# Performance work log

Measured on AMD Instinct MI355X. Metric: run time of the kernel, lower is better.

The kernel has to match this reference:

```python
import jax, jax.numpy as jnp
import numpy as np

N = 100000   # nodes
E = 1600000  # edges (before self-loops)
IN, HID, OUT = 256, 128, 64
NEG_SLOPE = 0.2  # PyG GATConv default


def setup_inputs() -> dict:
    key = jax.random.key(0)
    ks = jax.random.split(key, 12)
    s = 0.05
    return {
        "x": jax.random.normal(ks[0], (N, IN), jnp.float32),
        "edge_index": jax.random.randint(ks[1], (2, E), 0, N, dtype=jnp.int32),
        "W1": jax.random.normal(ks[2], (IN, HID), jnp.float32) * s,
        "a1_src": jax.random.normal(ks[3], (HID,), jnp.float32) * s,
        "a1_dst": jax.random.normal(ks[4], (HID,), jnp.float32) * s,
        "b1": jnp.zeros((HID,), jnp.float32),
        "W2": jax.random.normal(ks[5], (HID, OUT), jnp.float32) * s,
        "a2_src": jax.random.normal(ks[6], (OUT,), jnp.float32) * s,
        "a2_dst": jax.random.normal(ks[7], (OUT,), jnp.float32) * s,
        "b2": jnp.zeros((OUT,), jnp.float32),
    }


def _gat_conv(x, src, dst, W, a_src, a_dst, b):
    """Single-head PyG GATConv (concat=True, heads=1), self-loops already in src/dst."""
    h = x @ W                                   # [N, F]
    alpha_s = h @ a_src                         # [N]
    alpha_d = h @ a_dst                         # [N]
    e = jax.nn.leaky_relu(alpha_s[src] + alpha_d[dst], NEG_SLOPE)  # [E+N]
    # segment softmax over edges grouped by destination node
    m = jax.ops.segment_max(e, dst, num_segments=N)                # [N]
    ex = jnp.exp(e - m[dst])
    denom = jax.ops.segment_sum(ex, dst, num_segments=N)           # [N]
    coef = ex / denom[dst]                                         # [E+N]
    out = jax.ops.segment_sum(h[src] * coef[:, None], dst, num_segments=N)
    return out + b


def reference(x, edge_index, W1, a1_src, a1_dst, b1, W2, a2_src, a2_dst, b2):
    loops = jnp.arange(N, dtype=edge_index.dtype)
    src = jnp.concatenate([edge_index[0], loops])
    dst = jnp.concatenate([edge_index[1], loops])
    h = _gat_conv(x, src, dst, W1, a1_src, a1_dst, b1)
    h = jax.nn.relu(h)
    # dropout is identity at inference (training=False)
    out = _gat_conv(h, src, dst, W2, a2_src, a2_dst, b2)
    return out
```

## Files before the change

kernel.cpp:

```cpp
#include <hip/hip_runtime.h>
#include <hip/hip_bf16.h>
#include <cstdint>

#define N_NODES 100000
#define N_EDGES 1600000
#define F_IN 256
#define F_HID 128
#define F_OUT 64
#define NEG_SLOPE 0.2f

#define BSH 7
#define NB 782
#define CAP 3072
#define CAPS 3072
#define NBLK_E 256

typedef __attribute__((ext_vector_type(8))) short bf16x8;
typedef __attribute__((ext_vector_type(4))) float f32x4;

__device__ __forceinline__ ushort f2bf(float f) {
  uint u = __float_as_uint(f);
  u += 0x7fffu + ((u >> 16) & 1u);
  return (ushort)(u >> 16);
}
__device__ __forceinline__ float bf2f(ushort s) {
  return __uint_as_float(((uint)s) << 16);
}
__device__ __forceinline__ uint pack2(float a, float b) {
  return (uint)f2bf(a) | ((uint)f2bf(b) << 16);
}

__global__ void wprep_kernel(const float* __restrict__ W, ushort* __restrict__ Wt,
                             int K, int Ncol) {
  int i = blockIdx.x * blockDim.x + threadIdx.x;
  if (i < K * Ncol) {
    int k = i / Ncol, c = i % Ncol;
    Wt[(size_t)c * K + k] = f2bf(W[i]);
  }
}

template <int BN, int K, bool AF32>
__global__ __launch_bounds__(256) void gemm_mfma(
    const void* __restrict__ Ap, const ushort* __restrict__ Bt,
    ushort* __restrict__ Cb, const float* __restrict__ a_src,
    const float* __restrict__ a_dst, float* __restrict__ as_,
    float* __restrict__ ad_, int M) {
  constexpr int CT = BN / 16;
  __shared__ __align__(16) ushort Alds[128 * 32];
  __shared__ __align__(16) ushort Blds[BN * 32];
  const int tid = threadIdx.x;
  const int wave = tid >> 6, lane = tid & 63;
  const int lr = lane & 15, lq = lane >> 4;
  const int gm0 = blockIdx.x * 128;

  f32x4 acc[2][CT];
#pragma unroll
  for (int a = 0; a < 2; ++a)
#pragma unroll
    for (int b = 0; b < CT; ++b)
#pragma unroll
      for (int e = 0; e < 4; ++e) acc[a][b][e] = 0.f;

  for (int kt = 0; kt < K; kt += 32) {
#pragma unroll
    for (int i = 0; i < 2; ++i) {
      int sid = i * 256 + tid;
      int row = sid >> 2, q = sid & 3;
      int gm = gm0 + row;
      uint4 w = make_uint4(0u, 0u, 0u, 0u);
      if (gm < M) {
        if (AF32) {
          const float* s = (const float*)Ap + (size_t)gm * K + kt + q * 8;
          float4 u = *(const float4*)s;
          float4 v = *(const float4*)(s + 4);
          w.x = pack2(u.x, u.y); w.y = pack2(u.z, u.w);
          w.z = pack2(v.x, v.y); w.w = pack2(v.z, v.w);
        } else {
          w = *(const uint4*)((const ushort*)Ap + (size_t)gm * K + kt + q * 8);
        }
      }
      int phys = row * 4 + (q ^ ((row >> 2) & 3));
      *(uint4*)&Alds[phys * 8] = w;
    }
#pragma unroll
    for (int i = 0; i < BN * 4 / 256; ++i) {
      int sid = i * 256 + tid;
      int row = sid >> 2, q = sid & 3;
      uint4 w = *(const uint4*)(Bt + (size_t)row * K + kt + q * 8);
      int phys = row * 4 + (q ^ ((row >> 2) & 3));
      *(uint4*)&Blds[phys * 8] = w;
    }
    __syncthreads();

    bf16x8 af[2], bfr[CT];
#pragma unroll
    for (int rt = 0; rt < 2; ++rt) {
      int r = wave * 32 + rt * 16 + lr;
      af[rt] = *(const bf16x8*)&Alds[(r * 4 + (lq ^ ((r >> 2) & 3))) * 8];
    }
#pragma unroll
    for (int c = 0; c < CT; ++c) {
      int r = c * 16 + lr;
      bfr[c] = *(const bf16x8*)&Blds[(r * 4 + (lq ^ ((r >> 2) & 3))) * 8];
    }
#pragma unroll
    for (int rt = 0; rt < 2; ++rt)
#pragma unroll
      for (int c = 0; c < CT; ++c)
        acc[rt][c] = __builtin_amdgcn_mfma_f32_16x16x32_bf16(af[rt], bfr[c], acc[rt][c], 0, 0, 0);
    __syncthreads();
  }

#pragma unroll
  for (int rt = 0; rt < 2; ++rt)
#pragma unroll
    for (int ri = 0; ri < 4; ++ri) {
      int gr = gm0 + wave * 32 + rt * 16 + lq * 4 + ri;
      if (gr < M) {
#pragma unroll
        for (int c = 0; c < CT; ++c)
          Cb[(size_t)gr * BN + c * 16 + lr] = f2bf(acc[rt][c][ri]);
      }
    }

  float avs[CT], avd[CT];
#pragma unroll
  for (int c = 0; c < CT; ++c) {
    avs[c] = a_src[c * 16 + lr];
    avd[c] = a_dst[c * 16 + lr];
  }
#pragma unroll
  for (int rt = 0; rt < 2; ++rt)
#pragma unroll
    for (int ri = 0; ri < 4; ++ri) {
      int gr = gm0 + wave * 32 + rt * 16 + lq * 4 + ri;
      float s = 0.f, d = 0.f;
#pragma unroll
      for (int c = 0; c < CT; ++c) {
        float hv = acc[rt][c][ri];
        s += hv * avs[c];
        d += hv * avd[c];
      }
#pragma unroll
      for (int off = 1; off < 16; off <<= 1) {
        s += __shfl_xor(s, off);
        d += __shfl_xor(d, off);
      }
      if (gr < M && lr == 0) {
        as_[gr] = s;
        ad_[gr] = d;
      }
    }
}

__global__ __launch_bounds__(256) void ehist_kernel(const int* __restrict__ dst,
                                                    int* __restrict__ hist_blk) {
  __shared__ int h[NB];
  for (int t = threadIdx.x; t < NB; t += 256) h[t] = 0;
  __syncthreads();
  const int per = (N_EDGES + NBLK_E - 1) / NBLK_E;
  const int e0 = blockIdx.x * per;
  const int e1 = min(e0 + per, N_EDGES);
  for (int i = e0 + threadIdx.x; i < e1; i += 256)
    atomicAdd(&h[dst[i] >> BSH], 1);
  __syncthreads();
  for (int t = threadIdx.x; t < NB; t += 256)
    hist_blk[blockIdx.x * NB + t] = h[t];
}

__global__ __launch_bounds__(NBLK_E) void escan_kernel(int* __restrict__ hist_blk,
                                                       int* __restrict__ btotal) {
  __shared__ int sh[NBLK_E];
  const int j = blockIdx.x, t = threadIdx.x;
  int v = hist_blk[t * NB + j];
  sh[t] = v;
  __syncthreads();
  for (int off = 1; off < NBLK_E; off <<= 1) {
    int x = (t >= off) ? sh[t - off] : 0;
    __syncthreads();
    sh[t] += x;
    __syncthreads();
  }
  hist_blk[t * NB + j] = sh[t] - v;
  if (t == NBLK_E - 1) btotal[j] = sh[NBLK_E - 1];
}

__global__ __launch_bounds__(256) void escatter_kernel(
    const int* __restrict__ src, const int* __restrict__ dst,
    const int* __restrict__ hist_blk, uint* __restrict__ staged) {
  __shared__ int cur[NB];
  for (int t = threadIdx.x; t < NB; t += 256)
    cur[t] = hist_blk[blockIdx.x * NB + t];
  __syncthreads();
  const int per = (N_EDGES + NBLK_E - 1) / NBLK_E;
  const int e0 = blockIdx.x * per;
  const int e1 = min(e0 + per, N_EDGES);
  for (int i = e0 + threadIdx.x; i < e1; i += 256) {
    int d = dst[i];
    int b = d >> BSH;
    int p = atomicAdd(&cur[b], 1);
    if (p < CAPS)
      staged[(size_t)b * CAPS + p] = ((uint)src[i] << BSH) | (uint)(d & ((1 << BSH) - 1));
  }
}

__global__ __launch_bounds__(256) void fine_kernel(
    const uint* __restrict__ staged, const int* __restrict__ btotal,
    int* __restrict__ counts, int* __restrict__ offs, int* __restrict__ csr_src) {
  __shared__ int hist[128];
  __shared__ int cur[128];
  const int b = blockIdx.x, t = threadIdx.x;
  const int n0 = b << BSH;
  const int nn = min(128, N_NODES - n0);
  if (t < 128) hist[t] = 0;
  __syncthreads();
  const int ce = min(btotal[b], CAPS);
  const uint* sp = staged + (size_t)b * CAPS;
  for (int i = t; i < ce; i += 256)
    atomicAdd(&hist[sp[i] & 127], 1);
  __syncthreads();
  int v = 0;
  if (t < 128) {
    v = (t < nn) ? hist[t] + 1 : 0;
    cur[t] = v;
  }
  __syncthreads();
  for (int off = 1; off < 128; off <<= 1) {
    int x = 0;
    if (t < 128 && t >= off) x = cur[t - off];
    __syncthreads();
    if (t < 128) cur[t] += x;
    __syncthreads();
  }
  int excl = (t < 128) ? cur[t] - v : 0;
  __syncthreads();
  if (t < nn) {
    counts[n0 + t] = v;
    offs[n0 + t] = b * CAP + excl;
    csr_src[b * CAP + excl] = n0 + t;
    cur[t] = excl + 1;
  }
  __syncthreads();
  for (int i = t; i < ce; i += 256) {
    uint e = sp[i];
    int p = atomicAdd(&cur[e & 127], 1);
    csr_src[b * CAP + p] = (int)(e >> BSH);
  }
}

template <int C, bool RELU, bool OUTBF>
__global__ __launch_bounds__(256) void agg_kernel(
    const ushort* __restrict__ h, const float* __restrict__ as_,
    const float* __restrict__ ad_, const int* __restrict__ offs,
    const int* __restrict__ counts, const int* __restrict__ csr_src,
    const float* __restrict__ bias, void* __restrict__ outp, int M) {
  int wid = (int)((blockIdx.x * (size_t)blockDim.x + threadIdx.x) >> 6);
  int lane = threadIdx.x & 63;
  if (wid >= M) return;
  const int start = offs[wid];
  const int cnt = counts[wid];
  const float adn = ad_[wid];

  float m = -3.402823e38f, ssum = 0.f;
  int sj0 = 0;
  float e0 = -3.402823e38f;
  for (int j = lane; j < cnt; j += 64) {
    int sj = csr_src[start + j];
    float e = as_[sj] + adn;
    e = (e >= 0.f) ? e : NEG_SLOPE * e;
    if (j < 64) { sj0 = sj; e0 = e; }
    float mn = fmaxf(m, e);
    ssum = ssum * __expf(m - mn) + __expf(e - mn);
    m = mn;
  }
#pragma unroll
  for (int off = 32; off; off >>= 1) {
    float mo = __shfl_xor(m, off), so = __shfl_xor(ssum, off);
    float mn = fmaxf(m, mo);
    ssum = ssum * __expf(m - mn) + so * __expf(mo - mn);
    m = mn;
  }
  const float inv = 1.0f / ssum;

  float2 acc = make_float2(0.f, 0.f);
  const int half = lane >> 5;
  const int cl = lane & 31;

  for (int j0 = 0; j0 < cnt; j0 += 64) {
    int j = j0 + lane;
    int sj;
    float pj;
    if (j0 == 0) {
      sj = sj0;
      pj = __expf(e0 - m) * inv;
    } else {
      sj = 0;
      pj = 0.f;
      if (j < cnt) {
        sj = csr_src[start + j];
        float e = as_[sj] + adn;
        e = (e >= 0.f) ? e : NEG_SLOPE * e;
        pj = __expf(e - m) * inv;
      }
    }
    int c2 = min(64, cnt - j0);
    int jj = 0;
    if (C == 128) {
      for (; jj + 16 <= c2; jj += 16) {
        uint vv[16];
        float pp[16];
#pragma unroll
        for (int q = 0; q < 16; ++q) {
          int sq = __builtin_amdgcn_readlane(sj, jj + q);
          pp[q] = __uint_as_float((uint)__builtin_amdgcn_readlane((int)__float_as_uint(pj), jj + q));
          vv[q] = *((const uint*)(h + (size_t)sq * C) + lane);
        }
#pragma unroll
        for (int q = 0; q < 16; ++q) {
          acc.x = fmaf(pp[q], bf2f((ushort)(vv[q] & 0xffffu)), acc.x);
          acc.y = fmaf(pp[q], bf2f((ushort)(vv[q] >> 16)), acc.y);
        }
      }
      for (; jj + 4 <= c2; jj += 4) {
        uint vv[4];
        float pp[4];
#pragma unroll
        for (int q = 0; q < 4; ++q) {
          int sq = __builtin_amdgcn_readlane(sj, jj + q);
          pp[q] = __uint_as_float((uint)__builtin_amdgcn_readlane((int)__float_as_uint(pj), jj + q));
          vv[q] = *((const uint*)(h + (size_t)sq * C) + lane);
        }
#pragma unroll
        for (int q = 0; q < 4; ++q) {
          acc.x = fmaf(pp[q], bf2f((ushort)(vv[q] & 0xffffu)), acc.x);
          acc.y = fmaf(pp[q], bf2f((ushort)(vv[q] >> 16)), acc.y);
        }
      }
      for (; jj < c2; ++jj) {
        int sq = __builtin_amdgcn_readlane(sj, jj);
        float pq = __uint_as_float((uint)__builtin_amdgcn_readlane((int)__float_as_uint(pj), jj));
        uint v = *((const uint*)(h + (size_t)sq * C) + lane);
        acc.x = fmaf(pq, bf2f((ushort)(v & 0xffffu)), acc.x);
        acc.y = fmaf(pq, bf2f((ushort)(v >> 16)), acc.y);
      }
    } else {
      const uint* h32 = (const uint*)h;
      for (; jj + 16 <= c2; jj += 16) {
        uint vv[8];
        float pp[8];
#pragma unroll
        for (int q = 0; q < 8; ++q) {
          int idx = jj + 2 * q + half;
          int sq = __shfl(sj, idx);
          pp[q] = __shfl(pj, idx);
          vv[q] = h32[(size_t)sq * (C / 2) + cl];
        }
#pragma unroll
        for (int q = 0; q < 8; ++q) {
          acc.x = fmaf(pp[q], bf2f((ushort)(vv[q] & 0xffffu)), acc.x);
          acc.y = fmaf(pp[q], bf2f((ushort)(vv[q] >> 16)), acc.y);
        }
      }
      for (; jj < c2; jj += 2) {
        int idx = jj + half;
        int idc = min(idx, c2 - 1);
        int sq = __shfl(sj, idc);
        float pq = __shfl(pj, idc);
        if (idx >= c2) pq = 0.f;
        uint v = h32[(size_t)sq * (C / 2) + cl];
        acc.x = fmaf(pq, bf2f((ushort)(v & 0xffffu)), acc.x);
        acc.y = fmaf(pq, bf2f((ushort)(v >> 16)), acc.y);
      }
    }
  }

  if (C == 128) {
    float r0 = acc.x + bias[2 * lane];
    float r1 = acc.y + bias[2 * lane + 1];
    if (RELU) {
      r0 = fmaxf(r0, 0.f);
      r1 = fmaxf(r1, 0.f);
    }
    if (OUTBF)
      ((uint*)outp)[(size_t)wid * (C / 2) + lane] = pack2(r0, r1);
    else
      ((float2*)outp)[(size_t)wid * (C / 2) + lane] = make_float2(r0, r1);
  } else {
    acc.x += __shfl_xor(acc.x, 32);
    acc.y += __shfl_xor(acc.y, 32);
    if (lane < 32) {
      float r0 = acc.x + bias[2 * cl];
      float r1 = acc.y + bias[2 * cl + 1];
      if (RELU) {
        r0 = fmaxf(r0, 0.f);
        r1 = fmaxf(r1, 0.f);
      }
      if (OUTBF)
        ((uint*)outp)[(size_t)wid * (C / 2) + cl] = pack2(r0, r1);
      else
        ((float2*)outp)[(size_t)wid * (C / 2) + cl] = make_float2(r0, r1);
    }
  }
}

extern "C" void kernel_launch(void* const* d_in, const int* in_sizes, int n_in,
                              void* d_out, int out_size, void* d_ws, size_t ws_size,
                              hipStream_t stream) {
  const float* x = (const float*)d_in[0];
  const int* ei = (const int*)d_in[1];
  const float* W1 = (const float*)d_in[2];
  const float* a1s = (const float*)d_in[3];
  const float* a1d = (const float*)d_in[4];
  const float* b1 = (const float*)d_in[5];
  const float* W2 = (const float*)d_in[6];
  const float* a2s = (const float*)d_in[7];
  const float* a2d = (const float*)d_in[8];
  const float* b2 = (const float*)d_in[9];
  float* out = (float*)d_out;

  const int* esrc = ei;
  const int* edst = ei + N_EDGES;

  char* ws = (char*)d_ws;
  size_t off = 0;
  auto alloc = [&](size_t bytes) {
    size_t o = off;
    off = (off + bytes + 255) & ~(size_t)255;
    return o;
  };
  ushort* h1b = (ushort*)(ws + alloc((size_t)N_NODES * F_HID * 2));
  ushort* hrb = (ushort*)(ws + alloc((size_t)N_NODES * F_HID * 2));
  ushort* h2b = (ushort*)(ws + alloc((size_t)N_NODES * F_OUT * 2));
  float* as1 = (float*)(ws + alloc((size_t)N_NODES * 4));
  float* ad1 = (float*)(ws + alloc((size_t)N_NODES * 4));
  float* as2 = (float*)(ws + alloc((size_t)N_NODES * 4));
  float* ad2 = (float*)(ws + alloc((size_t)N_NODES * 4));
  int* counts = (int*)(ws + alloc((size_t)N_NODES * 4));
  int* offs = (int*)(ws + alloc((size_t)N_NODES * 4));
  int* hist_blk = (int*)(ws + alloc((size_t)NBLK_E * NB * 4));
  int* btotal = (int*)(ws + alloc((size_t)NB * 4));
  uint* staged = (uint*)(ws + alloc((size_t)NB * CAPS * 4));
  int* csr_src = (int*)(ws + alloc((size_t)NB * CAP * 4));
  ushort* W1t = (ushort*)(ws + alloc((size_t)F_IN * F_HID * 2));
  ushort* W2t = (ushort*)(ws + alloc((size_t)F_HID * F_OUT * 2));

  ehist_kernel<<<NBLK_E, 256, 0, stream>>>(edst, hist_blk);
  escan_kernel<<<NB, NBLK_E, 0, stream>>>(hist_blk, btotal);
  escatter_kernel<<<NBLK_E, 256, 0, stream>>>(esrc, edst, hist_blk, staged);
  fine_kernel<<<NB, 256, 0, stream>>>(staged, btotal, counts, offs, csr_src);

  wprep_kernel<<<(F_IN * F_HID + 255) / 256, 256, 0, stream>>>(W1, W1t, F_IN, F_HID);
  wprep_kernel<<<(F_HID * F_OUT + 255) / 256, 256, 0, stream>>>(W2, W2t, F_HID, F_OUT);

  gemm_mfma<F_HID, F_IN, true><<<(N_NODES + 127) / 128, 256, 0, stream>>>(
      x, W1t, h1b, a1s, a1d, as1, ad1, N_NODES);
  agg_kernel<F_HID, true, true><<<(N_NODES + 3) / 4, 256, 0, stream>>>(
      h1b, as1, ad1, offs, counts, csr_src, b1, hrb, N_NODES);

  gemm_mfma<F_OUT, F_HID, false><<<(N_NODES + 127) / 128, 256, 0, stream>>>(
      hrb, W2t, h2b, a2s, a2d, as2, ad2, N_NODES);
  agg_kernel<F_OUT, false, false><<<(N_NODES + 3) / 4, 256, 0, stream>>>(
      h2b, as2, ad2, offs, counts, csr_src, b2, out, N_NODES);
}
```

Measured before the change: 401.6 us.

## Fuse all stages into one cooperative persistent kernel with grid syncs

Replaces ten separate kernel launches with a single cooperative persistent kernel that walks each stage with a grid-stride loop and separates stages with grid.sync. The first GEMM is also overlapped with the edge histogram in one combined stage. GEMM tiles shrink from 128 to 64 rows so the kernel fits four blocks per CU. This removes launch gaps and tail effects between stages, at the cost of grid-wide barriers, register pressure from the merged code, and possibly lower occupancy in the aggregation phases.

```diff
diff --git a/kernel.cpp b/kernel.cpp
--- a/kernel.cpp
+++ b/kernel.cpp
@@ -1,6 +1,9 @@
 #include <hip/hip_runtime.h>
 #include <hip/hip_bf16.h>
+#include <hip/hip_cooperative_groups.h>
 #include <cstdint>
+
+namespace cg = cooperative_groups;
 
 #define N_NODES 100000
 #define N_EDGES 1600000
@@ -14,9 +17,28 @@
 #define CAP 3072
 #define CAPS 3072
 #define NBLK_E 256
+#define NT1 1563
+#define NAGG 25000
 
 typedef __attribute__((ext_vector_type(8))) short bf16x8;
 typedef __attribute__((ext_vector_type(4))) float f32x4;
+
+constexpr size_t AL(size_t x) { return (x + 255) & ~(size_t)255; }
+constexpr size_t OFF_H1B = 0;
+constexpr size_t OFF_HRB = OFF_H1B + AL((size_t)N_NODES * F_HID * 2);
+constexpr size_t OFF_H2B = OFF_HRB + AL((size_t)N_NODES * F_HID * 2);
+constexpr size_t OFF_AS1 = OFF_H2B + AL((size_t)N_NODES * F_OUT * 2);
+constexpr size_t OFF_AD1 = OFF_AS1 + AL((size_t)N_NODES * 4);
+constexpr size_t OFF_AS2 = OFF_AD1 + AL((size_t)N_NODES * 4);
+constexpr size_t OFF_AD2 = OFF_AS2 + AL((size_t)N_NODES * 4);
+constexpr size_t OFF_CNT = OFF_AD2 + AL((size_t)N_NODES * 4);
+constexpr size_t OFF_OFF = OFF_CNT + AL((size_t)N_NODES * 4);
+constexpr size_t OFF_HB  = OFF_OFF + AL((size_t)N_NODES * 4);
+constexpr size_t OFF_BT  = OFF_HB + AL((size_t)NBLK_E * NB * 4);
+constexpr size_t OFF_STG = OFF_BT + AL((size_t)NB * 4);
+constexpr size_t OFF_CSR = OFF_STG + AL((size_t)NB * CAPS * 4);
+constexpr size_t OFF_W1T = OFF_CSR + AL((size_t)NB * CAP * 4);
+constexpr size_t OFF_W2T = OFF_W1T + AL((size_t)F_IN * F_HID * 2);
 
 __device__ __forceinline__ ushort f2bf(float f) {
   uint u = __float_as_uint(f);
@@ -30,45 +52,32 @@
   return (uint)f2bf(a) | ((uint)f2bf(b) << 16);
 }
 
-__global__ void wprep_kernel(const float* __restrict__ W, ushort* __restrict__ Wt,
-                             int K, int Ncol) {
-  int i = blockIdx.x * blockDim.x + threadIdx.x;
-  if (i < K * Ncol) {
-    int k = i / Ncol, c = i % Ncol;
-    Wt[(size_t)c * K + k] = f2bf(W[i]);
-  }
-}
-
 template <int BN, int K, bool AF32>
-__global__ __launch_bounds__(256) void gemm_mfma(
-    const void* __restrict__ Ap, const ushort* __restrict__ Bt,
-    ushort* __restrict__ Cb, const float* __restrict__ a_src,
-    const float* __restrict__ a_dst, float* __restrict__ as_,
-    float* __restrict__ ad_, int M) {
+__device__ void gemm_tile(int tile, const void* __restrict__ Ap,
+                          const ushort* __restrict__ Bt, ushort* __restrict__ Cb,
+                          const float* __restrict__ a_src, const float* __restrict__ a_dst,
+                          float* __restrict__ as_, float* __restrict__ ad_,
+                          char* smem, int tid) {
   constexpr int CT = BN / 16;
-  __shared__ __align__(16) ushort Alds[128 * 32];
-  __shared__ __align__(16) ushort Blds[BN * 32];
-  const int tid = threadIdx.x;
+  ushort* Alds = (ushort*)smem;
+  ushort* Blds = ((ushort*)smem) + 64 * 32;
   const int wave = tid >> 6, lane = tid & 63;
   const int lr = lane & 15, lq = lane >> 4;
-  const int gm0 = blockIdx.x * 128;
-
-  f32x4 acc[2][CT];
-#pragma unroll
-  for (int a = 0; a < 2; ++a)
-#pragma unroll
-    for (int b = 0; b < CT; ++b)
-#pragma unroll
-      for (int e = 0; e < 4; ++e) acc[a][b][e] = 0.f;
-
+  const int gm0 = tile * 64;
+
+  f32x4 acc[CT];
+#pragma unroll
+  for (int c = 0; c < CT; ++c)
+#pragma unroll
+    for (int e = 0; e < 4; ++e) acc[c][e] = 0.f;
+
+  __syncthreads();
   for (int kt = 0; kt < K; kt += 32) {
-#pragma unroll
-    for (int i = 0; i < 2; ++i) {
-      int sid = i * 256 + tid;
-      int row = sid >> 2, q = sid & 3;
+    {
+      int row = tid >> 2, q = tid & 3;
       int gm = gm0 + row;
       uint4 w = make_uint4(0u, 0u, 0u, 0u);
-      if (gm < M) {
+      if (gm < N_NODES) {
         if (AF32) {
           const float* s = (const float*)Ap + (size_t)gm * K + kt + q * 8;
           float4 u = *(const float4*)s;
@@ -92,11 +101,10 @@
     }
     __syncthreads();
 
-    bf16x8 af[2], bfr[CT];
-#pragma unroll
-    for (int rt = 0; rt < 2; ++rt) {
-      int r = wave * 32 + rt * 16 + lr;
-      af[rt] = *(const bf16x8*)&Alds[(r * 4 + (lq ^ ((r >> 2) & 3))) * 8];
+    bf16x8 af, bfr[CT];
+    {
+      int r = wave * 16 + lr;
+      af = *(const bf16x8*)&Alds[(r * 4 + (lq ^ ((r >> 2) & 3))) * 8];
     }
 #pragma unroll
     for (int c = 0; c < CT; ++c) {
@@ -104,24 +112,20 @@
       bfr[c] = *(const bf16x8*)&Blds[(r * 4 + (lq ^ ((r >> 2) & 3))) * 8];
     }
 #pragma unroll
-    for (int rt = 0; rt < 2; ++rt)
+    for (int c = 0; c < CT; ++c)
+      acc[c] = __builtin_amdgcn_mfma_f32_16x16x32_bf16(af, bfr[c], acc[c], 0, 0, 0);
+    __syncthreads();
+  }
+
+#pragma unroll
+  for (int ri = 0; ri < 4; ++ri) {
+    int gr = gm0 + wave * 16 + lq * 4 + ri;
+    if (gr < N_NODES) {
 #pragma unroll
       for (int c = 0; c < CT; ++c)
-        acc[rt][c] = __builtin_amdgcn_mfma_f32_16x16x32_bf16(af[rt], bfr[c], acc[rt][c], 0, 0, 0);
-    __syncthreads();
-  }
-
-#pragma unroll
-  for (int rt = 0; rt < 2; ++rt)
-#pragma unroll
-    for (int ri = 0; ri < 4; ++ri) {
-      int gr = gm0 + wave * 32 + rt * 16 + lq * 4 + ri;
-      if (gr < M) {
-#pragma unroll
-        for (int c = 0; c < CT; ++c)
-          Cb[(size_t)gr * BN + c * 16 + lr] = f2bf(acc[rt][c][ri]);
-      }
-    }
+        Cb[(size_t)gr * BN + c * 16 + lr] = f2bf(acc[c][ri]);
+    }
+  }
 
   float avs[CT], avd[CT];
 #pragma unroll
@@ -130,48 +134,43 @@
     avd[c] = a_dst[c * 16 + lr];
   }
 #pragma unroll
-  for (int rt = 0; rt < 2; ++rt)
-#pragma unroll
-    for (int ri = 0; ri < 4; ++ri) {
-      int gr = gm0 + wave * 32 + rt * 16 + lq * 4 + ri;
-      float s = 0.f, d = 0.f;
-#pragma unroll
-      for (int c = 0; c < CT; ++c) {
-        float hv = acc[rt][c][ri];
-        s += hv * avs[c];
-        d += hv * avd[c];
-      }
-#pragma unroll
-      for (int off = 1; off < 16; off <<= 1) {
-        s += __shfl_xor(s, off);
-        d += __shfl_xor(d, off);
-      }
-      if (gr < M && lr == 0) {
-        as_[gr] = s;
-        ad_[gr] = d;
-      }
-    }
-}
-
-__global__ __launch_bounds__(256) void ehist_kernel(const int* __restrict__ dst,
-                                                    int* __restrict__ hist_blk) {
-  __shared__ int h[NB];
-  for (int t = threadIdx.x; t < NB; t += 256) h[t] = 0;
+  for (int ri = 0; ri < 4; ++ri) {
+    int gr = gm0 + wave * 16 + lq * 4 + ri;
+    float s = 0.f, d = 0.f;
+#pragma unroll
+    for (int c = 0; c < CT; ++c) {
+      s += acc[c][ri] * avs[c];
+      d += acc[c][ri] * avd[c];
+    }
+#pragma unroll
+    for (int off = 1; off < 16; off <<= 1) {
+      s += __shfl_xor(s, off);
+      d += __shfl_xor(d, off);
+    }
+    if (gr < N_NODES && lr == 0) {
+      as_[gr] = s;
+      ad_[gr] = d;
+    }
+  }
+}
+
+__device__ void ehist_unit(int c, const int* __restrict__ edst,
+                           int* __restrict__ hist_blk, char* smem, int t) {
+  int* h = (int*)smem;
+  __syncthreads();
+  for (int i = t; i < NB; i += 256) h[i] = 0;
   __syncthreads();
   const int per = (N_EDGES + NBLK_E - 1) / NBLK_E;
-  const int e0 = blockIdx.x * per;
-  const int e1 = min(e0 + per, N_EDGES);
-  for (int i = e0 + threadIdx.x; i < e1; i += 256)
-    atomicAdd(&h[dst[i] >> BSH], 1);
-  __syncthreads();
-  for (int t = threadIdx.x; t < NB; t += 256)
-    hist_blk[blockIdx.x * NB + t] = h[t];
-}
-
-__global__ __launch_bounds__(NBLK_E) void escan_kernel(int* __restrict__ hist_blk,
-                                                       int* __restrict__ btotal) {
-  __shared__ int sh[NBLK_E];
-  const int j = blockIdx.x, t = threadIdx.x;
+  const int e0 = c * per, e1 = min(e0 + per, N_EDGES);
+  for (int i = e0 + t; i < e1; i += 256) atomicAdd(&h[edst[i] >> BSH], 1);
+  __syncthreads();
+  for (int i = t; i < NB; i += 256) hist_blk[c * NB + i] = h[i];
+}
+
+__device__ void escan_unit(int j, int* __restrict__ hist_blk,
+                           int* __restrict__ btotal, char* smem, int t) {
+  int* sh = (int*)smem;
+  __syncthreads();
   int v = hist_blk[t * NB + j];
   sh[t] = v;
   __syncthreads();
@@ -185,17 +184,17 @@
   if (t == NBLK_E - 1) btotal[j] = sh[NBLK_E - 1];
 }
 
-__global__ __launch_bounds__(256) void escatter_kernel(
-    const int* __restrict__ src, const int* __restrict__ dst,
-    const int* __restrict__ hist_blk, uint* __restrict__ staged) {
-  __shared__ int cur[NB];
-  for (int t = threadIdx.x; t < NB; t += 256)
-    cur[t] = hist_blk[blockIdx.x * NB + t];
+__device__ void escatter_unit(int c, const int* __restrict__ src,
+                              const int* __restrict__ dst,
+                              const int* __restrict__ hist_blk,
+                              uint* __restrict__ staged, char* smem, int t) {
+  int* cur = (int*)smem;
+  __syncthreads();
+  for (int i = t; i < NB; i += 256) cur[i] = hist_blk[c * NB + i];
   __syncthreads();
   const int per = (N_EDGES + NBLK_E - 1) / NBLK_E;
-  const int e0 = blockIdx.x * per;
-  const int e1 = min(e0 + per, N_EDGES);
-  for (int i = e0 + threadIdx.x; i < e1; i += 256) {
+  const int e0 = c * per, e1 = min(e0 + per, N_EDGES);
+  for (int i = e0 + t; i < e1; i += 256) {
     int d = dst[i];
     int b = d >> BSH;
     int p = atomicAdd(&cur[b], 1);
@@ -204,20 +203,20 @@
   }
 }
 
-__global__ __launch_bounds__(256) void fine_kernel(
-    const uint* __restrict__ staged, const int* __restrict__ btotal,
-    int* __restrict__ counts, int* __restrict__ offs, int* __restrict__ csr_src) {
-  __shared__ int hist[128];
-  __shared__ int cur[128];
-  const int b = blockIdx.x, t = threadIdx.x;
+__device__ void fine_unit(int b, const uint* __restrict__ staged,
+                          const int* __restrict__ btotal, int* __restrict__ counts,
+                          int* __restrict__ offs, int* __restrict__ csr_src,
+                          char* smem, int t) {
+  int* hist = (int*)smem;
+  int* cur = hist + 128;
   const int n0 = b << BSH;
   const int nn = min(128, N_NODES - n0);
+  __syncthreads();
   if (t < 128) hist[t] = 0;
   __syncthreads();
   const int ce = min(btotal[b], CAPS);
   const uint* sp = staged + (size_t)b * CAPS;
-  for (int i = t; i < ce; i += 256)
-    atomicAdd(&hist[sp[i] & 127], 1);
+  for (int i = t; i < ce; i += 256) atomicAdd(&hist[sp[i] & 127], 1);
   __syncthreads();
   int v = 0;
   if (t < 128) {
@@ -249,14 +248,12 @@
 }
 
 template <int C, bool RELU, bool OUTBF>
-__global__ __launch_bounds__(256) void agg_kernel(
-    const ushort* __restrict__ h, const float* __restrict__ as_,
-    const float* __restrict__ ad_, const int* __restrict__ offs,
-    const int* __restrict__ counts, const int* __restrict__ csr_src,
-    const float* __restrict__ bias, void* __restrict__ outp, int M) {
-  int wid = (int)((blockIdx.x * (size_t)blockDim.x + threadIdx.x) >> 6);
-  int lane = threadIdx.x & 63;
-  if (wid >= M) return;
+__device__ void agg_node(int wid, int lane, const ushort* __restrict__ h,
+                         const float* __restrict__ as_, const float* __restrict__ ad_,
+                         const int* __restrict__ offs, const int* __restrict__ counts,
+                         const int* __restrict__ csr_src, const float* __restrict__ bias,
+                         void* __restrict__ outp) {
+  if (wid >= N_NODES) return;
   const int start = offs[wid];
   const int cnt = counts[wid];
   const float adn = ad_[wid];
@@ -403,6 +400,81 @@
   }
 }
 
+__global__ __launch_bounds__(256, 4) void mega_kernel(
+    const float* __restrict__ x, const int* __restrict__ ei,
+    const float* __restrict__ W1, const float* __restrict__ a1s,
+    const float* __restrict__ a1d, const float* __restrict__ b1,
+    const float* __restrict__ W2, const float* __restrict__ a2s,
+    const float* __restrict__ a2d, const float* __restrict__ b2,
+    float* __restrict__ out, char* __restrict__ ws) {
+  __shared__ __align__(16) char smem[12288];
+  cg::grid_group grid = cg::this_grid();
+  const int tid = threadIdx.x;
+  const int bid = blockIdx.x;
+  const int nblk = gridDim.x;
+  const int wave = tid >> 6, lane = tid & 63;
+
+  const int* esrc = ei;
+  const int* edst = ei + N_EDGES;
+  ushort* h1b = (ushort*)(ws + OFF_H1B);
+  ushort* hrb = (ushort*)(ws + OFF_HRB);
+  ushort* h2b = (ushort*)(ws + OFF_H2B);
+  float* as1 = (float*)(ws + OFF_AS1);
+  float* ad1 = (float*)(ws + OFF_AD1);
+  float* as2 = (float*)(ws + OFF_AS2);
+  float* ad2 = (float*)(ws + OFF_AD2);
+  int* counts = (int*)(ws + OFF_CNT);
+  int* offs = (int*)(ws + OFF_OFF);
+  int* hist_blk = (int*)(ws + OFF_HB);
+  int* btotal = (int*)(ws + OFF_BT);
+  uint* staged = (uint*)(ws + OFF_STG);
+  int* csr = (int*)(ws + OFF_CSR);
+  ushort* W1t = (ushort*)(ws + OFF_W1T);
+  ushort* W2t = (ushort*)(ws + OFF_W2T);
+
+  for (int i = bid * 256 + tid; i < F_IN * F_HID; i += nblk * 256) {
+    int k = i / F_HID, c = i % F_HID;
+    W1t[c * F_IN + k] = f2bf(W1[i]);
+  }
+  for (int i = bid * 256 + tid; i < F_HID * F_OUT; i += nblk * 256) {
+    int k = i / F_OUT, c = i % F_OUT;
+    W2t[c * F_HID + k] = f2bf(W2[i]);
+  }
+  grid.sync();
+
+  for (int u = bid; u < NT1 + NBLK_E; u += nblk) {
+    if (u < NT1)
+      gemm_tile<F_HID, F_IN, true>(u, x, W1t, h1b, a1s, a1d, as1, ad1, smem, tid);
+    else
+      ehist_unit(u - NT1, edst, hist_blk, smem, tid);
+  }
+  grid.sync();
+
+  for (int u = bid; u < NB; u += nblk) escan_unit(u, hist_blk, btotal, smem, tid);
+  grid.sync();
+
+  for (int u = bid; u < NBLK_E; u += nblk)
+    escatter_unit(u, esrc, edst, hist_blk, staged, smem, tid);
+  grid.sync();
+
+  for (int u = bid; u < NB; u += nblk)
+    fine_unit(u, staged, btotal, counts, offs, csr, smem, tid);
+  grid.sync();
+
+  for (int u = bid; u < NAGG; u += nblk)
+    agg_node<F_HID, true, true>(u * 4 + wave, lane, h1b, as1, ad1, offs, counts,
+                                csr, b1, hrb);
+  grid.sync();
+
+  for (int u = bid; u < NT1; u += nblk)
+    gemm_tile<F_OUT, F_HID, false>(u, hrb, W2t, h2b, a2s, a2d, as2, ad2, smem, tid);
+  grid.sync();
+
+  for (int u = bid; u < NAGG; u += nblk)
+    agg_node<F_OUT, false, false>(u * 4 + wave, lane, h2b, as2, ad2, offs, counts,
+                                  csr, b2, out);
+}
+
 extern "C" void kernel_launch(void* const* d_in, const int* in_sizes, int n_in,
                               void* d_out, int out_size, void* d_ws, size_t ws_size,
                               hipStream_t stream) {
@@ -417,48 +489,17 @@
   const float* a2d = (const float*)d_in[8];
   const float* b2 = (const float*)d_in[9];
   float* out = (float*)d_out;
-
-  const int* esrc = ei;
-  const int* edst = ei + N_EDGES;
-
   char* ws = (char*)d_ws;
-  size_t off = 0;
-  auto alloc = [&](size_t bytes) {
-    size_t o = off;
-    off = (off + bytes + 255) & ~(size_t)255;
-    return o;
-  };
-  ushort* h1b = (ushort*)(ws + alloc((size_t)N_NODES * F_HID * 2));
-  ushort* hrb = (ushort*)(ws + alloc((size_t)N_NODES * F_HID * 2));
-  ushort* h2b = (ushort*)(ws + alloc((size_t)N_NODES * F_OUT * 2));
-  float* as1 = (float*)(ws + alloc((size_t)N_NODES * 4));
-  float* ad1 = (float*)(ws + alloc((size_t)N_NODES * 4));
-  float* as2 = (float*)(ws + alloc((size_t)N_NODES * 4));
-  float* ad2 = (float*)(ws + alloc((size_t)N_NODES * 4));
-  int* counts = (int*)(ws + alloc((size_t)N_NODES * 4));
-  int* offs = (int*)(ws + alloc((size_t)N_NODES * 4));
-  int* hist_blk = (int*)(ws + alloc((size_t)NBLK_E * NB * 4));
-  int* btotal = (int*)(ws + alloc((size_t)NB * 4));
-  uint* staged = (uint*)(ws + alloc((size_t)NB * CAPS * 4));
-  int* csr_src = (int*)(ws + alloc((size_t)NB * CAP * 4));
-  ushort* W1t = (ushort*)(ws + alloc((size_t)F_IN * F_HID * 2));
-  ushort* W2t = (ushort*)(ws + alloc((size_t)F_HID * F_OUT * 2));
-
-  ehist_kernel<<<NBLK_E, 256, 0, stream>>>(edst, hist_blk);
-  escan_kernel<<<NB, NBLK_E, 0, stream>>>(hist_blk, btotal);
-  escatter_kernel<<<NBLK_E, 256, 0, stream>>>(esrc, edst, hist_blk, staged);
-  fine_kernel<<<NB, 256, 0, stream>>>(staged, btotal, counts, offs, csr_src);
-
-  wprep_kernel<<<(F_IN * F_HID + 255) / 256, 256, 0, stream>>>(W1, W1t, F_IN, F_HID);
-  wprep_kernel<<<(F_HID * F_OUT + 255) / 256, 256, 0, stream>>>(W2, W2t, F_HID, F_OUT);
-
-  gemm_mfma<F_HID, F_IN, true><<<(N_NODES + 127) / 128, 256, 0, stream>>>(
-      x, W1t, h1b, a1s, a1d, as1, ad1, N_NODES);
-  agg_kernel<F_HID, true, true><<<(N_NODES + 3) / 4, 256, 0, stream>>>(
-      h1b, as1, ad1, offs, counts, csr_src, b1, hrb, N_NODES);
-
-  gemm_mfma<F_OUT, F_HID, false><<<(N_NODES + 127) / 128, 256, 0, stream>>>(
-      hrb, W2t, h2b, a2s, a2d, as2, ad2, N_NODES);
-  agg_kernel<F_OUT, false, false><<<(N_NODES + 3) / 4, 256, 0, stream>>>(
-      h2b, as2, ad2, offs, counts, csr_src, b2, out, N_NODES);
-}
+
+  int maxb = 0;
+  if (hipOccupancyMaxActiveBlocksPerMultiprocessor(
+          &maxb, (const void*)mega_kernel, 256, 0) != hipSuccess || maxb <= 0)
+    maxb = 4;
+  if (maxb > 4) maxb = 4;
+  dim3 grid(maxb * 256), block(256);
+
+  void* args[] = {(void*)&x,   (void*)&ei,  (void*)&W1,  (void*)&a1s,
+                  (void*)&a1d, (void*)&b1,  (void*)&W2,  (void*)&a2s,
+                  (void*)&a2d, (void*)&b2,  (void*)&out, (void*)&ws};
+  hipLaunchCooperativeKernel((const void*)mega_kernel, grid, block, args, 0, stream);
+}
```

Result: slower. 1.024 ms (+155.1%).
